# Kernel optimization log

Measured on AMD Instinct MI355X. Metric: run time of the kernel, lower is better.

## Reference

```python
import jax, jax.numpy as jnp
import numpy as np

WS = 7       # window size
SHIFT = 3    # shift size (ws // 2)
NH = 8       # num heads


def _make_swin_mask(Hp, Wp, ws, shift):
    # Standard Swin attn mask for shifted windows: (nW, ws*ws, ws*ws)
    img = np.zeros((Hp, Wp), dtype=np.float32)
    cnt = 0
    for hs in (slice(0, -ws), slice(-ws, -shift), slice(-shift, None)):
        for wsl in (slice(0, -ws), slice(-ws, -shift), slice(-shift, None)):
            img[hs, wsl] = cnt
            cnt += 1
    mw = img.reshape(Hp // ws, ws, Wp // ws, ws).transpose(0, 2, 1, 3).reshape(-1, ws * ws)
    diff = mw[:, None, :] - mw[:, :, None]
    return jnp.asarray(np.where(diff != 0, -100.0, 0.0).astype(np.float32))


def setup_inputs() -> dict:
    key = jax.random.key(0)
    ks = jax.random.split(key, 5)
    B, H, W, C = 8, 128, 128, 256
    pad = (WS - H % WS) % WS
    Hp, Wp = H + pad, W + pad  # 133, 133
    x = jax.random.normal(ks[0], (B, H * W, C), dtype=jnp.float32)
    qkv_w = jax.random.normal(ks[1], (3 * C, C), dtype=jnp.float32) * 0.02
    qkv_b = jax.random.normal(ks[2], (3 * C,), dtype=jnp.float32) * 0.02
    proj_w = jax.random.normal(ks[3], (C, C), dtype=jnp.float32) * 0.02
    proj_b = jax.random.normal(ks[4], (C,), dtype=jnp.float32) * 0.02
    mask_matrix = _make_swin_mask(Hp, Wp, WS, SHIFT)
    return {"x": x, "qkv_w": qkv_w, "qkv_b": qkv_b, "proj_w": proj_w,
            "proj_b": proj_b, "mask_matrix": mask_matrix, "H": H, "W": W}


def reference(x, qkv_w, qkv_b, proj_w, proj_b, mask_matrix, H, W):
    B, N, C = x.shape
    hd = C // NH
    scale = hd ** -0.5
    xg = x.reshape(B, H, W, C)
    pad_r = (WS - W % WS) % WS
    pad_b = (WS - H % WS) % WS
    xg = jnp.pad(xg, ((0, 0), (0, pad_b), (0, pad_r), (0, 0)))
    Hp, Wp = H + pad_b, W + pad_r
    xg = jnp.roll(xg, (-SHIFT, -SHIFT), axis=(1, 2))
    h, w = Hp // WS, Wp // WS
    nW = h * w
    wsws = WS * WS
    # window partition -> (B*nW, wsws, C)
    xw = xg.reshape(B, h, WS, w, WS, C).transpose(0, 1, 3, 2, 4, 5).reshape(B * nW, wsws, C)
    qkv = xw @ qkv_w.T + qkv_b                       # (B*nW, wsws, 3C)
    qkv = qkv.reshape(B * nW, wsws, 3, NH, hd).transpose(2, 0, 3, 1, 4)
    q, k, v = qkv[0], qkv[1], qkv[2]                 # (B*nW, NH, wsws, hd)
    attn = jnp.einsum('bhqd,bhkd->bhqk', q, k) * scale
    attn = attn.reshape(B, nW, NH, wsws, wsws) + mask_matrix[None, :, None]
    attn = jax.nn.softmax(attn, axis=-1).reshape(B * nW, NH, wsws, wsws)
    out = jnp.einsum('bhqk,bhkd->bhqd', attn, v)
    out = out.transpose(0, 2, 1, 3).reshape(B * nW, wsws, C)
    out = out @ proj_w.T + proj_b
    # window reverse -> (B, Hp, Wp, C)
    out = out.reshape(B, h, w, WS, WS, C).transpose(0, 1, 3, 2, 4, 5).reshape(B, Hp, Wp, C)
    out = jnp.roll(out, (SHIFT, SHIFT), axis=(1, 2))
    return out[:, :H, :W, :].reshape(B, N, C)
```

## Files before the change

### kernel.cpp

```cpp
#include <hip/hip_runtime.h>
#include <hip/hip_bf16.h>
#include <cstdint>
#include <cstddef>

#define WS7    7
#define NHEADS 8
#define HD     32
#define CDIM   256
#define HP     133
#define NWY    19
#define NWIN   361
#define BATCH  8
#define HIMG   128
#define TOK    49
#define MTOK   64
#define SHIFT3 3

typedef __attribute__((ext_vector_type(8))) short short8;
typedef __attribute__((ext_vector_type(4))) short short4v;
typedef __attribute__((ext_vector_type(4))) float f32x4;

#define XROWB  528
#define VROW   76
#define VT_OFF 33792
#define SMEM_BYTES (VT_OFF + 256*VROW*2)

#define QS      0.25505653712988137f
#define MASKL2 -144.26950408889634f

__device__ __forceinline__ short f2bf(float f) {
  union { float f; uint32_t u; } v; v.f = f;
  uint32_t r = v.u + 0x7FFFu + ((v.u >> 16) & 1u);
  return (short)(r >> 16);
}

__device__ __forceinline__ uint32_t pk2(float a, float b) {
  union { __hip_bfloat162 h; uint32_t u; } cv;
  cv.h = __float22bfloat162_rn(float2{a, b});
  return cv.u;
}

#if defined(__has_builtin)
#if __has_builtin(__builtin_amdgcn_exp2f)
#define EXP2F __builtin_amdgcn_exp2f
#else
#define EXP2F exp2f
#endif
#else
#define EXP2F exp2f
#endif

#if defined(__has_builtin)
#if __has_builtin(__builtin_amdgcn_mfma_f32_16x16x16bf16_1k)
#define HAVE_MFMA16 1
#endif
#endif

__device__ __forceinline__ f32x4 mfma16(short4v a, short4v b, f32x4 c) {
#ifdef HAVE_MFMA16
  return __builtin_amdgcn_mfma_f32_16x16x16bf16_1k(a, b, c, 0, 0, 0);
#else
  asm("v_mfma_f32_16x16x16_bf16 %0, %1, %2, %0" : "+v"(c) : "v"(a), "v"(b));
  return c;
#endif
}

__device__ __forceinline__ int regcode(int c) { return (c < 126) ? 0 : ((c < 130) ? 1 : 2); }

__global__ void cvt_weights(const float* __restrict__ qkv_w, const float* __restrict__ proj_w,
                            short* __restrict__ qkvw_bf, short* __restrict__ projw_bf) {
  int stride = gridDim.x * blockDim.x;
  int i0 = blockIdx.x * blockDim.x + threadIdx.x;
  for (int i = i0; i < 768 * 256; i += stride) qkvw_bf[i] = f2bf(qkv_w[i]);
  for (int i = i0; i < 256 * 256; i += stride) projw_bf[i] = f2bf(proj_w[i]);
}

__global__ __launch_bounds__(512, 4) void swin_fused(
    const float* __restrict__ x, const short* __restrict__ qkvw,
    const float* __restrict__ qkv_b, const short* __restrict__ projw,
    const float* __restrict__ proj_b, float* __restrict__ out)
{
  extern __shared__ char smem[];
  const int tid  = threadIdx.x;
  const int wave = tid >> 6;
  const int lane = tid & 63;
  const int lg   = lane >> 4;
  const int ln   = lane & 15;
  const int blk  = blockIdx.x;
  const int b    = blk / NWIN;
  const int wdx  = blk - b * NWIN;
  const int wy   = wdx / NWY;
  const int wx   = wdx - wy * NWY;

  {
    const int c4 = lane;
#pragma unroll
    for (int it = 0; it < 8; ++it) {
      int r = 8 * it + wave;
      uint2 v = make_uint2(0u, 0u);
      if (r < TOK) {
        int ty = r / WS7, tx = r - WS7 * (r / WS7);
        int sh = wy * WS7 + ty + SHIFT3; if (sh >= HP) sh -= HP;
        int sw = wx * WS7 + tx + SHIFT3; if (sw >= HP) sw -= HP;
        if (sh < HIMG && sw < HIMG) {
          const float4 f = *reinterpret_cast<const float4*>(
              x + (((size_t)b * (HIMG * HIMG) + sh * HIMG + sw) * CDIM + c4 * 4));
          v = make_uint2(pk2(f.x, f.y), pk2(f.z, f.w));
        }
      }
      *reinterpret_cast<uint2*>(smem + r * XROWB + c4 * 8) = v;
    }
  }
  __syncthreads();

  const int h = wave;
  const int qcol = h * HD;
  const int kcol = 256 + h * HD;
  const int vcol = 512 + h * HD;

  short4v qf[2][4], kf[2][4];

  {
    f32x4 acc[2][4];
#pragma unroll
    for (int ct = 0; ct < 2; ++ct)
#pragma unroll
      for (int tt = 0; tt < 4; ++tt) acc[ct][tt] = (f32x4){0, 0, 0, 0};
#pragma unroll 2
    for (int ks = 0; ks < 8; ++ks) {
      const int k0 = ks * 32 + lg * 8;
      short8 xb[4];
#pragma unroll
      for (int tt = 0; tt < 4; ++tt)
        xb[tt] = *reinterpret_cast<const short8*>(smem + (16 * tt + ln) * XROWB + k0 * 2);
      short8 w[2];
#pragma unroll
      for (int ct = 0; ct < 2; ++ct)
        w[ct] = *reinterpret_cast<const short8*>(qkvw + (size_t)(vcol + 16 * ct + ln) * CDIM + k0);
#pragma unroll
      for (int ct = 0; ct < 2; ++ct)
#pragma unroll
        for (int tt = 0; tt < 4; ++tt)
          acc[ct][tt] = __builtin_amdgcn_mfma_f32_16x16x32_bf16(w[ct], xb[tt], acc[ct][tt], 0, 0, 0);
    }
#pragma unroll
    for (int ct = 0; ct < 2; ++ct) {
      f32x4 bias = *reinterpret_cast<const f32x4*>(qkv_b + vcol + 16 * ct + 4 * lg);
#pragma unroll
      for (int tt = 0; tt < 4; ++tt) {
        uint32_t p01 = pk2(acc[ct][tt][0] + bias[0], acc[ct][tt][1] + bias[1]);
        uint32_t p23 = pk2(acc[ct][tt][2] + bias[2], acc[ct][tt][3] + bias[3]);
        int row0 = h * HD + 16 * ct + 4 * lg;
        int col  = 16 * tt + ln;
        char* base = smem + VT_OFF + (row0 * VROW + col) * 2;
        *reinterpret_cast<short*>(base)            = (short)(p01 & 0xFFFF);
        *reinterpret_cast<short*>(base + VROW * 2) = (short)(p01 >> 16);
        *reinterpret_cast<short*>(base + VROW * 4) = (short)(p23 & 0xFFFF);
        *reinterpret_cast<short*>(base + VROW * 6) = (short)(p23 >> 16);
      }
    }
  }

  {
    f32x4 acc[4][4];
#pragma unroll
    for (int c = 0; c < 4; ++c)
#pragma unroll
      for (int tt = 0; tt < 4; ++tt) acc[c][tt] = (f32x4){0, 0, 0, 0};
#pragma unroll 2
    for (int ks = 0; ks < 8; ++ks) {
      const int k0 = ks * 32 + lg * 8;
      short8 xb[4];
#pragma unroll
      for (int tt = 0; tt < 4; ++tt)
        xb[tt] = *reinterpret_cast<const short8*>(smem + (16 * tt + ln) * XROWB + k0 * 2);
      short8 wq[2], wk[2];
#pragma unroll
      for (int ct = 0; ct < 2; ++ct) {
        wq[ct] = *reinterpret_cast<const short8*>(qkvw + (size_t)(qcol + 16 * ct + ln) * CDIM + k0);
        wk[ct] = *reinterpret_cast<const short8*>(qkvw + (size_t)(kcol + 16 * ct + ln) * CDIM + k0);
      }
#pragma unroll
      for (int ct = 0; ct < 2; ++ct)
#pragma unroll
        for (int tt = 0; tt < 4; ++tt) {
          acc[ct][tt]     = __builtin_amdgcn_mfma_f32_16x16x32_bf16(wq[ct], xb[tt], acc[ct][tt], 0, 0, 0);
          acc[2 + ct][tt] = __builtin_amdgcn_mfma_f32_16x16x32_bf16(wk[ct], xb[tt], acc[2 + ct][tt], 0, 0, 0);
        }
    }
#pragma unroll
    for (int ct = 0; ct < 2; ++ct) {
      f32x4 bq = *reinterpret_cast<const f32x4*>(qkv_b + qcol + 16 * ct + 4 * lg);
      f32x4 bk = *reinterpret_cast<const f32x4*>(qkv_b + kcol + 16 * ct + 4 * lg);
#pragma unroll
      for (int tt = 0; tt < 4; ++tt) {
        float e0 = fmaf(acc[ct][tt][0], QS, bq[0] * QS);
        float e1 = fmaf(acc[ct][tt][1], QS, bq[1] * QS);
        float e2 = fmaf(acc[ct][tt][2], QS, bq[2] * QS);
        float e3 = fmaf(acc[ct][tt][3], QS, bq[3] * QS);
        union { uint2 u; short4v s; } cq;
        cq.u = make_uint2(pk2(e0, e1), pk2(e2, e3));
        qf[ct][tt] = cq.s;
        union { uint2 u; short4v s; } ck;
        ck.u = make_uint2(pk2(acc[2 + ct][tt][0] + bk[0], acc[2 + ct][tt][1] + bk[1]),
                          pk2(acc[2 + ct][tt][2] + bk[2], acc[2 + ct][tt][3] + bk[3]));
        kf[ct][tt] = ck.s;
      }
    }
  }
  __syncthreads();

  const bool bnd = (wy == NWY - 1) || (wx == NWY - 1);
#pragma unroll
  for (int qt = 0; qt < 4; ++qt) {
    f32x4 sq[4];
#pragma unroll
    for (int kt = 0; kt < 4; ++kt) sq[kt] = (f32x4){0, 0, 0, 0};
#pragma unroll
    for (int step = 0; step < 2; ++step)
#pragma unroll
      for (int kt = 0; kt < 4; ++kt)
        sq[kt] = mfma16(kf[step][kt], qf[step][qt], sq[kt]);

    int q = 16 * qt + ln;
    int qcode = 0;
    if (bnd) {
      int qy = q / WS7, qx = q - WS7 * (q / WS7);
      qcode = 3 * regcode(wy * WS7 + qy) + regcode(wx * WS7 + qx);
    }
    float sum = 0.f;
#pragma unroll
    for (int kt = 0; kt < 4; ++kt)
#pragma unroll
      for (int r = 0; r < 4; ++r) {
        int key = 16 * kt + 4 * lg + r;
        float v = sq[kt][r];
        if (bnd) {
          int ky = key / WS7, kx = key - WS7 * (key / WS7);
          int kc = 3 * regcode(wy * WS7 + ky) + regcode(wx * WS7 + kx);
          v += (kc != qcode) ? MASKL2 : 0.f;
        }
        if (key >= TOK) v = -1e30f;
        float e = EXP2F(v);
        sq[kt][r] = e; sum += e;
      }
    sum += __shfl_xor(sum, 16);
    sum += __shfl_xor(sum, 32);
    float inv = 1.0f / sum;

    short4v pf[4];
#pragma unroll
    for (int kt = 0; kt < 4; ++kt) {
      union { uint2 u; short4v sv; } cv;
      cv.u = make_uint2(pk2(sq[kt][0] * inv, sq[kt][1] * inv),
                        pk2(sq[kt][2] * inv, sq[kt][3] * inv));
      pf[kt] = cv.sv;
    }

    f32x4 o0 = (f32x4){0, 0, 0, 0};
    f32x4 o1 = (f32x4){0, 0, 0, 0};
#pragma unroll
    for (int kt = 0; kt < 4; ++kt) {
      int tok = 16 * kt + 4 * lg;
      short4v vb0 = *reinterpret_cast<const short4v*>(
          smem + VT_OFF + ((h * HD + 2 * ln) * VROW + tok) * 2);
      short4v vb1 = *reinterpret_cast<const short4v*>(
          smem + VT_OFF + ((h * HD + 2 * ln + 1) * VROW + tok) * 2);
      o0 = mfma16(pf[kt], vb0, o0);
      o1 = mfma16(pf[kt], vb1, o1);
    }

#pragma unroll
    for (int r = 0; r < 4; ++r) {
      int row = 16 * qt + 4 * lg + r;
      *reinterpret_cast<uint32_t*>(smem + row * XROWB + h * 64 + 4 * ln) = pk2(o0[r], o1[r]);
    }
  }
  __syncthreads();

  f32x4 pacc[4][2];
#pragma unroll
  for (int mt = 0; mt < 4; ++mt)
#pragma unroll
    for (int n2 = 0; n2 < 2; ++n2) pacc[mt][n2] = (f32x4){0, 0, 0, 0};
#pragma unroll 2
  for (int ks = 0; ks < 8; ++ks) {
    int k0 = ks * 32 + lg * 8;
    short8 afr[4];
#pragma unroll
    for (int mt = 0; mt < 4; ++mt)
      afr[mt] = *reinterpret_cast<const short8*>(smem + (16 * mt + ln) * XROWB + k0 * 2);
    short8 bfr[2];
#pragma unroll
    for (int n2 = 0; n2 < 2; ++n2)
      bfr[n2] = *reinterpret_cast<const short8*>(projw + (size_t)(h * HD + 16 * n2 + ln) * CDIM + k0);
#pragma unroll
    for (int n2 = 0; n2 < 2; ++n2)
#pragma unroll
      for (int mt = 0; mt < 4; ++mt)
        pacc[mt][n2] = __builtin_amdgcn_mfma_f32_16x16x32_bf16(afr[mt], bfr[n2], pacc[mt][n2], 0, 0, 0);
  }

  float pb0 = proj_b[h * HD + ln];
  float pb1 = proj_b[h * HD + 16 + ln];
#pragma unroll
  for (int mt = 0; mt < 4; ++mt)
#pragma unroll
    for (int r = 0; r < 4; ++r) {
      int t = 16 * mt + 4 * lg + r;
      if (t < TOK) {
        int ty = t / WS7, tx = t - WS7 * (t / WS7);
        int sh = wy * WS7 + ty + SHIFT3; if (sh >= HP) sh -= HP;
        int sw = wx * WS7 + tx + SHIFT3; if (sw >= HP) sw -= HP;
        if (sh < HIMG && sw < HIMG) {
          float* po = out + ((size_t)b * (HIMG * HIMG) + sh * HIMG + sw) * CDIM + h * HD + ln;
          po[0]  = pacc[mt][0][r] + pb0;
          po[16] = pacc[mt][1][r] + pb1;
        }
      }
    }
}

extern "C" void kernel_launch(void* const* d_in, const int* in_sizes, int n_in,
                              void* d_out, int out_size, void* d_ws, size_t ws_size,
                              hipStream_t stream) {
  const float* x      = (const float*)d_in[0];
  const float* qkv_w  = (const float*)d_in[1];
  const float* qkv_b  = (const float*)d_in[2];
  const float* proj_w = (const float*)d_in[3];
  const float* proj_b = (const float*)d_in[4];
  float* out          = (float*)d_out;

  short* qkvw_bf = (short*)d_ws;
  short* projw_bf = (short*)((char*)d_ws + 768 * 256 * 2);

  hipLaunchKernelGGL(cvt_weights, dim3(256), dim3(256), 0, stream,
                     qkv_w, proj_w, qkvw_bf, projw_bf);

  hipFuncSetAttribute((const void*)swin_fused,
                      hipFuncAttributeMaxDynamicSharedMemorySize, SMEM_BYTES);
  hipLaunchKernelGGL(swin_fused, dim3(BATCH * NWIN), dim3(512), SMEM_BYTES, stream,
                     x, qkvw_bf, qkv_b, projw_bf, proj_b, out);
}
```

Before: 241.2 us.

## Keep V in registers via identity-MFMA transpose instead of LDS V^T buffer

Computes V after Q/K and transposes the V tiles in registers by multiplying with an identity matrix through an MFMA, instead of writing V transposed into a separate LDS region. The transposed V fragments feed the P·V MFMAs directly, which removes the VT LDS buffer and its scattered 2-byte stores and reads. Shared memory per block shrinks, which may let more blocks reside per CU. In exchange it adds extra MFMAs, register pressure from holding tb, and output column ordering changes to match the new layout.

```diff
diff --git a/kernel.cpp b/kernel.cpp
--- a/kernel.cpp
+++ b/kernel.cpp
@@ -21,9 +21,7 @@
 typedef __attribute__((ext_vector_type(4))) float f32x4;
 
 #define XROWB  528
-#define VROW   76
-#define VT_OFF 33792
-#define SMEM_BYTES (VT_OFF + 256*VROW*2)
+#define SMEM_BYTES 33792
 
 #define QS      0.25505653712988137f
 #define MASKL2 -144.26950408889634f
@@ -121,47 +119,6 @@
   short4v qf[2][4], kf[2][4];
 
   {
-    f32x4 acc[2][4];
-#pragma unroll
-    for (int ct = 0; ct < 2; ++ct)
-#pragma unroll
-      for (int tt = 0; tt < 4; ++tt) acc[ct][tt] = (f32x4){0, 0, 0, 0};
-#pragma unroll 2
-    for (int ks = 0; ks < 8; ++ks) {
-      const int k0 = ks * 32 + lg * 8;
-      short8 xb[4];
-#pragma unroll
-      for (int tt = 0; tt < 4; ++tt)
-        xb[tt] = *reinterpret_cast<const short8*>(smem + (16 * tt + ln) * XROWB + k0 * 2);
-      short8 w[2];
-#pragma unroll
-      for (int ct = 0; ct < 2; ++ct)
-        w[ct] = *reinterpret_cast<const short8*>(qkvw + (size_t)(vcol + 16 * ct + ln) * CDIM + k0);
-#pragma unroll
-      for (int ct = 0; ct < 2; ++ct)
-#pragma unroll
-        for (int tt = 0; tt < 4; ++tt)
-          acc[ct][tt] = __builtin_amdgcn_mfma_f32_16x16x32_bf16(w[ct], xb[tt], acc[ct][tt], 0, 0, 0);
-    }
-#pragma unroll
-    for (int ct = 0; ct < 2; ++ct) {
-      f32x4 bias = *reinterpret_cast<const f32x4*>(qkv_b + vcol + 16 * ct + 4 * lg);
-#pragma unroll
-      for (int tt = 0; tt < 4; ++tt) {
-        uint32_t p01 = pk2(acc[ct][tt][0] + bias[0], acc[ct][tt][1] + bias[1]);
-        uint32_t p23 = pk2(acc[ct][tt][2] + bias[2], acc[ct][tt][3] + bias[3]);
-        int row0 = h * HD + 16 * ct + 4 * lg;
-        int col  = 16 * tt + ln;
-        char* base = smem + VT_OFF + (row0 * VROW + col) * 2;
-        *reinterpret_cast<short*>(base)            = (short)(p01 & 0xFFFF);
-        *reinterpret_cast<short*>(base + VROW * 2) = (short)(p01 >> 16);
-        *reinterpret_cast<short*>(base + VROW * 4) = (short)(p23 & 0xFFFF);
-        *reinterpret_cast<short*>(base + VROW * 6) = (short)(p23 >> 16);
-      }
-    }
-  }
-
-  {
     f32x4 acc[4][4];
 #pragma unroll
     for (int c = 0; c < 4; ++c)
@@ -208,6 +165,49 @@
       }
     }
   }
+
+  short4v tb[2][4];
+  {
+    f32x4 acc[2][4];
+#pragma unroll
+    for (int ct = 0; ct < 2; ++ct)
+#pragma unroll
+      for (int tt = 0; tt < 4; ++tt) acc[ct][tt] = (f32x4){0, 0, 0, 0};
+#pragma unroll 2
+    for (int ks = 0; ks < 8; ++ks) {
+      const int k0 = ks * 32 + lg * 8;
+      short8 xb[4];
+#pragma unroll
+      for (int tt = 0; tt < 4; ++tt)
+        xb[tt] = *reinterpret_cast<const short8*>(smem + (16 * tt + ln) * XROWB + k0 * 2);
+      short8 w[2];
+#pragma unroll
+      for (int ct = 0; ct < 2; ++ct)
+        w[ct] = *reinterpret_cast<const short8*>(qkvw + (size_t)(vcol + 16 * ct + ln) * CDIM + k0);
+#pragma unroll
+      for (int ct = 0; ct < 2; ++ct)
+#pragma unroll
+        for (int tt = 0; tt < 4; ++tt)
+          acc[ct][tt] = __builtin_amdgcn_mfma_f32_16x16x32_bf16(w[ct], xb[tt], acc[ct][tt], 0, 0, 0);
+    }
+    short4v idb;
+#pragma unroll
+    for (int j = 0; j < 4; ++j) idb[j] = (short)((ln == 4 * lg + j) ? 0x3F80 : 0);
+#pragma unroll
+    for (int ct = 0; ct < 2; ++ct) {
+      f32x4 bias = *reinterpret_cast<const f32x4*>(qkv_b + vcol + 16 * ct + 4 * lg);
+#pragma unroll
+      for (int tt = 0; tt < 4; ++tt) {
+        union { uint2 u; short4v s; } av;
+        av.u = make_uint2(pk2(acc[ct][tt][0] + bias[0], acc[ct][tt][1] + bias[1]),
+                          pk2(acc[ct][tt][2] + bias[2], acc[ct][tt][3] + bias[3]));
+        f32x4 t = mfma16(av.s, idb, (f32x4){0, 0, 0, 0});
+        union { uint2 u; short4v s; } tv;
+        tv.u = make_uint2(pk2(t[0], t[1]), pk2(t[2], t[3]));
+        tb[ct][tt] = tv.s;
+      }
+    }
+  }
   __syncthreads();
 
   const bool bnd = (wy == NWY - 1) || (wx == NWY - 1);
@@ -261,19 +261,15 @@
     f32x4 o1 = (f32x4){0, 0, 0, 0};
 #pragma unroll
     for (int kt = 0; kt < 4; ++kt) {
-      int tok = 16 * kt + 4 * lg;
-      short4v vb0 = *reinterpret_cast<const short4v*>(
-          smem + VT_OFF + ((h * HD + 2 * ln) * VROW + tok) * 2);
-      short4v vb1 = *reinterpret_cast<const short4v*>(
-          smem + VT_OFF + ((h * HD + 2 * ln + 1) * VROW + tok) * 2);
-      o0 = mfma16(pf[kt], vb0, o0);
-      o1 = mfma16(pf[kt], vb1, o1);
+      o0 = mfma16(pf[kt], tb[0][kt], o0);
+      o1 = mfma16(pf[kt], tb[1][kt], o1);
     }
 
 #pragma unroll
     for (int r = 0; r < 4; ++r) {
       int row = 16 * qt + 4 * lg + r;
-      *reinterpret_cast<uint32_t*>(smem + row * XROWB + h * 64 + 4 * ln) = pk2(o0[r], o1[r]);
+      *reinterpret_cast<short*>(smem + row * XROWB + (h * HD + ln) * 2)      = f2bf(o0[r]);
+      *reinterpret_cast<short*>(smem + row * XROWB + (h * HD + 16 + ln) * 2) = f2bf(o1[r]);
     }
   }
   __syncthreads();
```

Measured after the change: 271.7 us. 1.13x slower.
